# Performance work log

Hardware: AMD Instinct MI355X
Metric: run time of the kernel (lower is better)

The kernel has to match this reference:

```python
import jax, jax.numpy as jnp
import numpy as np

L, NH, D, FF, NL, NP = 6, 8, 256, 1024, 4, 4
HD = D // NH
B, Q0 = 4, 1000
SIZES = [(128, 128), (64, 64), (32, 32), (16, 16)]
KEEP_RATIO = 0.5


def _ln(x, w, b, eps=1e-5):
    mu = x.mean(-1, keepdims=True)
    var = ((x - mu) ** 2).mean(-1, keepdims=True)
    return (x - mu) * jax.lax.rsqrt(var + eps) * w + b


def _mha(q, k, v, in_w, in_b, out_w, out_b):
    # torch nn.MultiheadAttention (batch_first, eval mode => no dropout)
    Bq, Qn, _ = q.shape
    wq, wk, wv = jnp.split(in_w, 3, axis=0)
    bq, bk, bv = jnp.split(in_b, 3, axis=0)
    proj = lambda x, w, bb: (x @ w.T + bb).reshape(Bq, -1, NH, HD).transpose(0, 2, 1, 3)
    qh, kh, vh = proj(q, wq, bq), proj(k, wk, bk), proj(v, wv, bv)
    scores = jnp.einsum('bhqd,bhkd->bhqk', qh, kh) * (1.0 / np.float32(np.sqrt(HD)))
    a = jax.nn.softmax(scores, axis=-1)
    o = jnp.einsum('bhqk,bhkd->bhqd', a, vh).transpose(0, 2, 1, 3).reshape(Bq, Qn, D)
    return o @ out_w.T + out_b


def _bilinear(feat, grid):
    # feat [B,NH,HD,H,W]; grid [B,NH,Q,P,2] (x,y) in [-1,1]
    # matches F.grid_sample(mode='bilinear', padding_mode='zeros', align_corners=True)
    Bf, nh, hd, H, W = feat.shape
    gx = (grid[..., 0] + 1.0) * 0.5 * (W - 1)
    gy = (grid[..., 1] + 1.0) * 0.5 * (H - 1)
    x0, y0 = jnp.floor(gx), jnp.floor(gy)
    flat = feat.reshape(Bf, nh, hd, H * W)
    Qn, P = grid.shape[2], grid.shape[3]

    def corner(xi, yi, w):
        valid = (xi >= 0) & (xi <= W - 1) & (yi >= 0) & (yi <= H - 1)
        idx = (jnp.clip(yi, 0, H - 1).astype(jnp.int32) * W
               + jnp.clip(xi, 0, W - 1).astype(jnp.int32)).reshape(Bf, nh, Qn * P)
        vals = jnp.take_along_axis(flat, jnp.broadcast_to(idx[:, :, None, :], (Bf, nh, hd, Qn * P)), axis=3)
        vals = vals.reshape(Bf, nh, hd, Qn, P)
        return vals * (w * valid)[:, :, None]

    wx1, wy1 = gx - x0, gy - y0
    return (corner(x0, y0, (1 - wx1) * (1 - wy1)) + corner(x0 + 1, y0, wx1 * (1 - wy1))
            + corner(x0, y0 + 1, (1 - wx1) * wy1) + corner(x0 + 1, y0 + 1, wx1 * wy1))


def _msdeform(query, feats, ref, off_w, off_b, aw_w, aw_b, out_w, out_b):
    Bq, Qn, _ = query.shape
    off = jnp.tanh((query @ off_w.T + off_b).reshape(Bq, Qn, NH, NL, NP, 2))
    attn = jax.nn.softmax((query @ aw_w.T + aw_b).reshape(Bq, Qn, NH, NL * NP), axis=3)
    attn = attn.reshape(Bq, Qn, NH, NL, NP)
    ref_grid = ref * 2.0 - 1.0  # [B,Q,2]
    agg = 0.0
    for lvl, feat in enumerate(feats):
        fh = feat.reshape(Bq, NH, HD, feat.shape[2], feat.shape[3])
        grid = ref_grid[:, None, :, None, :] + off[:, :, :, lvl].transpose(0, 2, 1, 3, 4)  # [B,NH,Q,NP,2]
        sampled = _bilinear(fh, grid)                     # [B,NH,HD,Q,NP]
        w = attn[:, :, :, lvl].transpose(0, 2, 1, 3)      # [B,NH,Q,NP]
        agg = agg + (sampled * w[:, :, None]).sum(-1)     # [B,NH,HD,Q]
    out = agg.transpose(0, 3, 1, 2).reshape(Bq, Qn, D)
    return out @ out_w.T + out_b, attn


def setup_inputs() -> dict:
    key = jax.random.key(0)
    ks = iter(jax.random.split(key, 64))
    nrm = lambda shape, s=0.02: jax.random.normal(next(ks), shape, jnp.float32) * s
    inp = {
        'query_objects': nrm((B, Q0, D), 1.0),
        'query_embed': nrm((B, Q0, D), 1.0),
    }
    for i, (H, W) in enumerate(SIZES):
        inp[f'feat{i}'] = nrm((B, D, H, W), 1.0)
    inp.update(
        sa_in_w=nrm((L, 3 * D, D)), sa_in_b=jnp.zeros((L, 3 * D)),
        sa_out_w=nrm((L, D, D)), sa_out_b=jnp.zeros((L, D)),
        off_w=nrm((L, NH * NL * NP * 2, D)), off_b=nrm((L, NH * NL * NP * 2), 0.1),
        aw_w=nrm((L, NH * NL * NP, D)), aw_b=jnp.zeros((L, NH * NL * NP)),
        ca_out_w=nrm((L, D, D)), ca_out_b=jnp.zeros((L, D)),
        ff_w1=nrm((L, FF, D)), ff_b1=jnp.zeros((L, FF)),
        ff_w2=nrm((L, D, FF)), ff_b2=jnp.zeros((L, D)),
        nsa_w=jnp.ones((L, D)), nsa_b=jnp.zeros((L, D)),
        nca_w=jnp.ones((L, D)), nca_b=jnp.zeros((L, D)),
        nff_w=jnp.ones((L, D)), nff_b=jnp.zeros((L, D)),
        ref_w1=nrm((D, D)), ref_b1=jnp.zeros((D,)),
        ref_w2=nrm((2, D)), ref_b2=jnp.zeros((2,)),
        score_w=nrm((1, D)), score_b=jnp.zeros((1,)),
        refine_w=nrm((2, D)), refine_b=jnp.zeros((2,)),
    )
    return inp


def reference(query_objects, query_embed, feat0, feat1, feat2, feat3,
              sa_in_w, sa_in_b, sa_out_w, sa_out_b,
              off_w, off_b, aw_w, aw_b, ca_out_w, ca_out_b,
              ff_w1, ff_b1, ff_w2, ff_b2,
              nsa_w, nsa_b, nca_w, nca_b, nff_w, nff_b,
              ref_w1, ref_b1, ref_w2, ref_b2,
              score_w, score_b, refine_w, refine_b):
    feats = [feat0, feat1, feat2, feat3]
    out, q_embed = query_objects, query_embed
    h = jax.nn.relu(q_embed @ ref_w1.T + ref_b1)
    ref_points = jax.nn.sigmoid(h @ ref_w2.T + ref_b2)  # [B,Q,2]
    outputs, attns = [], []
    for i in range(L):
        sa_in = _ln(out, nsa_w[i], nsa_b[i])
        sa_out = _mha(sa_in + q_embed, sa_in + q_embed, sa_in,
                      sa_in_w[i], sa_in_b[i], sa_out_w[i], sa_out_b[i])
        out = out + sa_out
        ca_in = _ln(out, nca_w[i], nca_b[i])
        ca_out, attn = _msdeform(ca_in + q_embed, feats, ref_points,
                                 off_w[i], off_b[i], aw_w[i], aw_b[i], ca_out_w[i], ca_out_b[i])
        out = out + ca_out
        ff_in = _ln(out, nff_w[i], nff_b[i])
        out = out + (jax.nn.relu(ff_in @ ff_w1[i].T + ff_b1[i]) @ ff_w2[i].T + ff_b2[i])
        delta = jnp.tanh(out @ refine_w.T + refine_b) * 0.5
        ref_points = jnp.clip(ref_points + delta, 0.0, 1.0)
        outputs.append(out)
        attns.append(attn)
        if i < L - 1:
            Qn = out.shape[1]
            keep = max(16, int(Qn * KEEP_RATIO))
            scores = jax.nn.sigmoid((jax.lax.stop_gradient(out) @ score_w.T + score_b)[..., 0])
            _, idx = jax.lax.top_k(scores, keep)
            out = jnp.take_along_axis(out, idx[:, :, None], axis=1)
            q_embed = jnp.take_along_axis(q_embed, idx[:, :, None], axis=1)
            ref_points = jnp.take_along_axis(ref_points, idx[:, :, None], axis=1)
    return tuple(outputs) + tuple(attns)
```

## Files before the change

### kernel.cpp

```cpp
#include <hip/hip_runtime.h>
#include <hip/hip_bf16.h>

#define BB 4
#define DD 256

typedef unsigned long long u64;
typedef long long s64;
typedef unsigned int u32;

__device__ __forceinline__ float sigm(float x) { return 1.0f / (1.0f + expf(-x)); }

__global__ void k_ln(const float* __restrict__ x, const float* __restrict__ w,
                     const float* __restrict__ b, float* __restrict__ ln) {
    int row = blockIdx.x, tid = threadIdx.x;
    float v = x[(size_t)row * DD + tid];
    __shared__ float sred[4];
    float s = v;
#pragma unroll
    for (int o = 32; o > 0; o >>= 1) s += __shfl_down(s, o);
    if ((tid & 63) == 0) sred[tid >> 6] = s;
    __syncthreads();
    float mu = (sred[0] + sred[1] + sred[2] + sred[3]) * (1.0f / 256.0f);
    __syncthreads();
    float d = v - mu;
    float s2 = d * d;
#pragma unroll
    for (int o = 32; o > 0; o >>= 1) s2 += __shfl_down(s2, o);
    if ((tid & 63) == 0) sred[tid >> 6] = s2;
    __syncthreads();
    float var = (sred[0] + sred[1] + sred[2] + sred[3]) * (1.0f / 256.0f);
    float r = rsqrtf(var + 1e-5f);
    ln[(size_t)row * DD + tid] = d * r * w[tid] + b[tid];
}

template <int ACT, int RES>
__device__ __forceinline__ void gemm_core(float (*As)[16][64], float (*Ws)[16][64],
                                          const float* __restrict__ A, const float* __restrict__ Pe, int pe,
                                          const float* __restrict__ W, const float* __restrict__ bias,
                                          const float* __restrict__ Rm, float* __restrict__ C,
                                          float* __restrict__ C2,
                                          int M, int N, int K, int row0, int col0) {
    int tid = threadIdx.x;
    int tx = tid & 15, ty = tid >> 4;
    int lm = tid >> 2, lk = (tid & 3) * 4;
    float acc[4][4] = {{0.f}};
    int ar = row0 + lm;
    const float* Arow = A + (size_t)ar * K + lk;
    const float* Prow = pe ? (Pe + (size_t)ar * K + lk) : nullptr;
    const float* Wrow = W + (size_t)(col0 + lm) * K + lk;
    float4 av = make_float4(0.f, 0.f, 0.f, 0.f), wv;
    if (ar < M) {
        av = *(const float4*)(Arow);
        if (pe) { float4 pv = *(const float4*)(Prow); av.x += pv.x; av.y += pv.y; av.z += pv.z; av.w += pv.w; }
    }
    wv = *(const float4*)(Wrow);
    As[0][lk + 0][lm] = av.x; As[0][lk + 1][lm] = av.y; As[0][lk + 2][lm] = av.z; As[0][lk + 3][lm] = av.w;
    Ws[0][lk + 0][lm] = wv.x; Ws[0][lk + 1][lm] = wv.y; Ws[0][lk + 2][lm] = wv.z; Ws[0][lk + 3][lm] = wv.w;
    __syncthreads();
    int nb = K >> 4;
    for (int t = 0; t < nb; t++) {
        int cur = t & 1, nxt = cur ^ 1;
        bool more = (t + 1 < nb);
        if (more) {
            int k0 = (t + 1) << 4;
            av = make_float4(0.f, 0.f, 0.f, 0.f);
            if (ar < M) {
                av = *(const float4*)(Arow + k0);
                if (pe) { float4 pv = *(const float4*)(Prow + k0); av.x += pv.x; av.y += pv.y; av.z += pv.z; av.w += pv.w; }
            }
            wv = *(const float4*)(Wrow + k0);
        }
#pragma unroll
        for (int kk = 0; kk < 16; kk++) {
            float4 a = *(const float4*)&As[cur][kk][ty << 2];
            float4 w = *(const float4*)&Ws[cur][kk][tx << 2];
            acc[0][0] += a.x * w.x; acc[0][1] += a.x * w.y; acc[0][2] += a.x * w.z; acc[0][3] += a.x * w.w;
            acc[1][0] += a.y * w.x; acc[1][1] += a.y * w.y; acc[1][2] += a.y * w.z; acc[1][3] += a.y * w.w;
            acc[2][0] += a.z * w.x; acc[2][1] += a.z * w.y; acc[2][2] += a.z * w.z; acc[2][3] += a.z * w.w;
            acc[3][0] += a.w * w.x; acc[3][1] += a.w * w.y; acc[3][2] += a.w * w.z; acc[3][3] += a.w * w.w;
        }
        if (more) {
            As[nxt][lk + 0][lm] = av.x; As[nxt][lk + 1][lm] = av.y; As[nxt][lk + 2][lm] = av.z; As[nxt][lk + 3][lm] = av.w;
            Ws[nxt][lk + 0][lm] = wv.x; Ws[nxt][lk + 1][lm] = wv.y; Ws[nxt][lk + 2][lm] = wv.z; Ws[nxt][lk + 3][lm] = wv.w;
        }
        __syncthreads();
    }
#pragma unroll
    for (int i2 = 0; i2 < 4; i2++) {
        int r = row0 + (ty << 2) + i2;
        if (r >= M) continue;
        int cc = col0 + (tx << 2);
        float4 v;
        v.x = acc[i2][0] + bias[cc + 0];
        v.y = acc[i2][1] + bias[cc + 1];
        v.z = acc[i2][2] + bias[cc + 2];
        v.w = acc[i2][3] + bias[cc + 3];
        if (ACT == 1) { v.x = fmaxf(v.x, 0.f); v.y = fmaxf(v.y, 0.f); v.z = fmaxf(v.z, 0.f); v.w = fmaxf(v.w, 0.f); }
        if (RES == 1) {
            float4 rm = *(const float4*)(Rm + (size_t)r * N + cc);
            v.x += rm.x; v.y += rm.y; v.z += rm.z; v.w += rm.w;
        }
        *(float4*)(C + (size_t)r * N + cc) = v;
        if (C2) *(float4*)(C2 + (size_t)r * N + cc) = v;
    }
}

template <int ACT, int RES, int PE>
__global__ __launch_bounds__(256) void k_gemm(const float* __restrict__ A, const float* __restrict__ Pe,
                                              const float* __restrict__ W, const float* __restrict__ bias,
                                              const float* __restrict__ Rm, float* __restrict__ C,
                                              int M, int N, int K) {
    __shared__ float As[2][16][64];
    __shared__ float Ws[2][16][64];
    gemm_core<ACT, RES>(As, Ws, A, Pe, PE, W, bias, Rm, C, nullptr, M, N, K, blockIdx.y * 64, blockIdx.x * 64);
}

__global__ __launch_bounds__(256) void k_gemm_st2(const float* __restrict__ A, const float* __restrict__ W,
                                                  const float* __restrict__ bias, const float* __restrict__ Rm,
                                                  float* __restrict__ C, float* __restrict__ C2,
                                                  int M, int N, int K) {
    __shared__ float As[2][16][64];
    __shared__ float Ws[2][16][64];
    gemm_core<0, 1>(As, Ws, A, nullptr, 0, W, bias, Rm, C, C2, M, N, K, blockIdx.y * 64, blockIdx.x * 64);
}

__global__ __launch_bounds__(256) void k_gemm_qkv(const float* __restrict__ A, const float* __restrict__ Pe,
                                                  const float* __restrict__ Wqkv, const float* __restrict__ bqkv,
                                                  float* __restrict__ Cq, float* __restrict__ Ck, float* __restrict__ Cv,
                                                  int M, int K) {
    __shared__ float As[2][16][64];
    __shared__ float Ws[2][16][64];
    int z = blockIdx.z;
    const float* W = Wqkv + (size_t)z * 256 * K;
    const float* bias = bqkv + z * 256;
    float* C = (z == 0) ? Cq : (z == 1) ? Ck : Cv;
    gemm_core<0, 0>(As, Ws, A, Pe, (z < 2) ? 1 : 0, W, bias, nullptr, C, nullptr, M, 256, K,
                    blockIdx.y * 64, blockIdx.x * 64);
}

__global__ __launch_bounds__(256) void k_gemm_offaw(const float* __restrict__ A, const float* __restrict__ Pe,
                                                    const float* __restrict__ Woff, const float* __restrict__ boff,
                                                    const float* __restrict__ Waw, const float* __restrict__ baw,
                                                    float* __restrict__ Coff, float* __restrict__ Caw,
                                                    int M, int K) {
    __shared__ float As[2][16][64];
    __shared__ float Ws[2][16][64];
    int z = blockIdx.z;
    int N = (z == 0) ? 256 : 128;
    if ((int)(blockIdx.x * 64) >= N) return;
    gemm_core<0, 0>(As, Ws, A, Pe, 1, (z == 0) ? Woff : Waw, (z == 0) ? boff : baw, nullptr,
                    (z == 0) ? Coff : Caw, nullptr, M, N, K, blockIdx.y * 64, blockIdx.x * 64);
}

#define MHA_DOT8(SREG, JJ)                                                       \
    {                                                                            \
        _Pragma("unroll")                                                        \
        for (int u = 0; u < 8; u++) SREG[u] = 0.f;                               \
        _Pragma("unroll")                                                        \
        for (int c4 = 0; c4 < 8; c4++) {                                         \
            float q0 = qv[c4 * 4 + 0], q1 = qv[c4 * 4 + 1];                      \
            float q2 = qv[c4 * 4 + 2], q3 = qv[c4 * 4 + 3];                      \
            _Pragma("unroll")                                                    \
            for (int u = 0; u < 8; u++) {                                        \
                float4 k4 = *(const float4*)&Ks[(JJ) + u][c4 * 4];               \
                SREG[u] += q0 * k4.x; SREG[u] += q1 * k4.y;                      \
                SREG[u] += q2 * k4.z; SREG[u] += q3 * k4.w;                      \
            }                                                                    \
        }                                                                        \
    }

__global__ __launch_bounds__(64) void k_mha(const float* __restrict__ Qb, const float* __restrict__ Kb,
                                            const float* __restrict__ Vb, float* __restrict__ Ob, int Qn) {
    int bh = blockIdx.y;
    int b = bh >> 3, h = bh & 7;
    int lane = threadIdx.x;
    int qi = blockIdx.x * 64 + lane;
    __shared__ float Ks[64][36];
    __shared__ float Vs[64][36];
    float qv[32];
    float acc[32];
#pragma unroll
    for (int c = 0; c < 32; c++) acc[c] = 0.f;
    float m = -INFINITY, l = 0.f;
    const float scale = 0.17677669529663687f;
    bool active = qi < Qn;
    if (active) {
        const float4* qp = (const float4*)(Qb + ((size_t)(b * Qn + qi)) * DD + h * 32);
#pragma unroll
        for (int c4 = 0; c4 < 8; c4++) {
            float4 t = qp[c4];
            qv[c4 * 4 + 0] = t.x * scale; qv[c4 * 4 + 1] = t.y * scale;
            qv[c4 * 4 + 2] = t.z * scale; qv[c4 * 4 + 3] = t.w * scale;
        }
    } else {
#pragma unroll
        for (int c = 0; c < 32; c++) qv[c] = 0.f;
    }
    for (int k0 = 0; k0 < Qn; k0 += 64) {
        int nk = Qn - k0; if (nk > 64) nk = 64;
        if (lane < nk) {
            const float4* kp = (const float4*)(Kb + ((size_t)(b * Qn + k0 + lane)) * DD + h * 32);
            const float4* vp = (const float4*)(Vb + ((size_t)(b * Qn + k0 + lane)) * DD + h * 32);
#pragma unroll
            for (int c4 = 0; c4 < 8; c4++) {
                *(float4*)&Ks[lane][c4 * 4] = kp[c4];
                *(float4*)&Vs[lane][c4 * 4] = vp[c4];
            }
        }
        __syncthreads();
        int ng = nk >> 3;
        float scur[8], snxt[8];
        if (ng > 0) MHA_DOT8(scur, 0)
        for (int g = 0; g < ng; g++) {
            int jj = g << 3;
            bool morep = (g + 1 < ng);
            if (morep) MHA_DOT8(snxt, jj + 8)
            float mch[9];
            mch[0] = m;
#pragma unroll
            for (int u = 0; u < 8; u++) mch[u + 1] = fmaxf(mch[u], scur[u]);
            float e8[8];
#pragma unroll
            for (int u = 0; u < 8; u++) e8[u] = expf(fminf(mch[u] - scur[u], scur[u] - mch[u]));
            float sc8[8], p8[8];
#pragma unroll
            for (int u = 0; u < 8; u++) {
                bool gt = scur[u] > mch[u];
                sc8[u] = gt ? e8[u] : 1.0f;
                p8[u] = gt ? 1.0f : e8[u];
                l = l * sc8[u] + p8[u];
            }
            m = mch[8];
            float4 vc[8], vn[8];
#pragma unroll
            for (int c4 = 0; c4 < 8; c4++) vc[c4] = *(const float4*)&Vs[jj][c4 * 4];
#pragma unroll
            for (int u = 0; u < 8; u++) {
                if (u < 7) {
#pragma unroll
                    for (int c4 = 0; c4 < 8; c4++) vn[c4] = *(const float4*)&Vs[jj + u + 1][c4 * 4];
                }
                float sc = sc8[u], p = p8[u];
#pragma unroll
                for (int c4 = 0; c4 < 8; c4++) {
                    acc[c4 * 4 + 0] = acc[c4 * 4 + 0] * sc + p * vc[c4].x;
                    acc[c4 * 4 + 1] = acc[c4 * 4 + 1] * sc + p * vc[c4].y;
                    acc[c4 * 4 + 2] = acc[c4 * 4 + 2] * sc + p * vc[c4].z;
                    acc[c4 * 4 + 3] = acc[c4 * 4 + 3] * sc + p * vc[c4].w;
                }
                if (u < 7) {
#pragma unroll
                    for (int c4 = 0; c4 < 8; c4++) vc[c4] = vn[c4];
                }
            }
            if (morep) {
#pragma unroll
                for (int u = 0; u < 8; u++) scur[u] = snxt[u];
            }
        }
        for (int j = ng << 3; j < nk; j++) {
            float sv = 0.f;
#pragma unroll
            for (int c4 = 0; c4 < 8; c4++) {
                float4 k4 = *(const float4*)&Ks[j][c4 * 4];
                sv += qv[c4 * 4 + 0] * k4.x; sv += qv[c4 * 4 + 1] * k4.y;
                sv += qv[c4 * 4 + 2] * k4.z; sv += qv[c4 * 4 + 3] * k4.w;
            }
            float mn = fmaxf(m, sv);
            float e = expf(fminf(m - sv, sv - m));
            bool gt = sv > m;
            float sc = gt ? e : 1.0f;
            float p = gt ? 1.0f : e;
            l = l * sc + p;
            m = mn;
#pragma unroll
            for (int c4 = 0; c4 < 8; c4++) {
                float4 v4 = *(const float4*)&Vs[j][c4 * 4];
                acc[c4 * 4 + 0] = acc[c4 * 4 + 0] * sc + p * v4.x;
                acc[c4 * 4 + 1] = acc[c4 * 4 + 1] * sc + p * v4.y;
                acc[c4 * 4 + 2] = acc[c4 * 4 + 2] * sc + p * v4.z;
                acc[c4 * 4 + 3] = acc[c4 * 4 + 3] * sc + p * v4.w;
            }
        }
        __syncthreads();
    }
    if (active) {
        float inv = 1.0f / l;
        float* op = Ob + ((size_t)(b * Qn + qi)) * DD + h * 32;
#pragma unroll
        for (int c4 = 0; c4 < 8; c4++) {
            float4 o;
            o.x = acc[c4 * 4 + 0] * inv; o.y = acc[c4 * 4 + 1] * inv;
            o.z = acc[c4 * 4 + 2] * inv; o.w = acc[c4 * 4 + 3] * inv;
            *(float4*)(op + c4 * 4) = o;
        }
    }
}

__global__ __launch_bounds__(256) void k_trfeat(const float* __restrict__ in, float* __restrict__ out, int HH) {
    __shared__ float t[32][65];
    int bh = blockIdx.y;
    int b = bh >> 3, h = bh & 7;
    int s0 = blockIdx.x * 64;
    int tid = threadIdx.x;
    const float* ip = in + ((size_t)(b * 256 + h * 32)) * HH + s0;
#pragma unroll
    for (int i = 0; i < 8; i++) {
        int idx = i * 256 + tid;
        int c = idx >> 6, s = idx & 63;
        t[c][s] = ip[(size_t)c * HH + s];
    }
    __syncthreads();
    float* op = out + ((size_t)bh * HH + s0) * 32;
#pragma unroll
    for (int i = 0; i < 8; i++) {
        int idx = i * 256 + tid;
        int s = idx >> 5, c = idx & 31;
        op[(size_t)s * 32 + c] = t[c][s];
    }
}

__device__ __forceinline__ float d_samp(const float* fp, int W, int H, int x, int y) {
    if (x < 0 || x > W - 1 || y < 0 || y > H - 1) return 0.f;
    return fp[y * W + x];
}
__device__ __forceinline__ float d_bil(const float* fp, int W, int H, float gx, float gy) {
    float fx = (gx + 1.0f) * 0.5f * (float)(W - 1);
    float fy = (gy + 1.0f) * 0.5f * (float)(H - 1);
    float x0f = floorf(fx), y0f = floorf(fy);
    int x0 = (int)x0f, y0 = (int)y0f;
    float wx = fx - x0f, wy = fy - y0f;
    float v00 = d_samp(fp, W, H, x0, y0);
    float v10 = d_samp(fp, W, H, x0 + 1, y0);
    float v01 = d_samp(fp, W, H, x0, y0 + 1);
    float v11 = d_samp(fp, W, H, x0 + 1, y0 + 1);
    return v00 * (1.f - wx) * (1.f - wy) + v10 * wx * (1.f - wy) + v01 * (1.f - wx) * wy + v11 * wx * wy;
}
__device__ __forceinline__ float d_samp32(const float* fp, int W, int H, int x, int y) {
    if (x < 0 || x > W - 1 || y < 0 || y > H - 1) return 0.f;
    return fp[(size_t)(y * W + x) * 32];
}
__device__ __forceinline__ float d_bil32(const float* fp, int W, int H, float gx, float gy) {
    float fx = (gx + 1.0f) * 0.5f * (float)(W - 1);
    float fy = (gy + 1.0f) * 0.5f * (float)(H - 1);
    float x0f = floorf(fx), y0f = floorf(fy);
    int x0 = (int)x0f, y0 = (int)y0f;
    float wx = fx - x0f, wy = fy - y0f;
    float v00 = d_samp32(fp, W, H, x0, y0);
    float v10 = d_samp32(fp, W, H, x0 + 1, y0);
    float v01 = d_samp32(fp, W, H, x0, y0 + 1);
    float v11 = d_samp32(fp, W, H, x0 + 1, y0 + 1);
    return v00 * (1.f - wx) * (1.f - wy) + v10 * wx * (1.f - wy) + v01 * (1.f - wx) * wy + v11 * wx * wy;
}

template <int TR>
__global__ __launch_bounds__(256) void k_deform(const float* __restrict__ offL, const float* __restrict__ awL,
                                                const float* __restrict__ ref,
                                                const float* __restrict__ f0, const float* __restrict__ f1,
                                                const float* __restrict__ f2, const float* __restrict__ f3,
                                                float* __restrict__ caf, float* __restrict__ attn_out,
                                                int Qn) {
    int row = blockIdx.x;
    int b = row / Qn;
    int tid = threadIdx.x;
    __shared__ float attn_s[8][16];
    __shared__ float off_s[8][16][2];
    __shared__ float rxy[2];
    if (tid < 8) {
        int h = tid;
        const float* ap = awL + (size_t)row * 128 + h * 16;
        float mx = -INFINITY;
        float e[16];
#pragma unroll
        for (int j = 0; j < 16; j++) mx = fmaxf(mx, ap[j]);
        float ssum = 0.f;
#pragma unroll
        for (int j = 0; j < 16; j++) { e[j] = expf(ap[j] - mx); ssum += e[j]; }
        float inv = 1.0f / ssum;
        float* ao = attn_out + (size_t)row * 128 + h * 16;
#pragma unroll
        for (int j = 0; j < 16; j++) {
            float p = e[j] * inv;
            attn_s[h][j] = p;
            ao[j] = p;
        }
        const float* op = offL + (size_t)row * 256 + h * 32;
#pragma unroll
        for (int j = 0; j < 16; j++) {
            off_s[h][j][0] = tanhf(op[j * 2 + 0]);
            off_s[h][j][1] = tanhf(op[j * 2 + 1]);
        }
    }
    if (tid == 8) {
        rxy[0] = ref[(size_t)row * 2 + 0] * 2.f - 1.f;
        rxy[1] = ref[(size_t)row * 2 + 1] * 2.f - 1.f;
    }
    __syncthreads();
    int h = tid >> 5, c = tid & 31;
    float agg = 0.f;
#pragma unroll
    for (int l = 0; l < 4; l++) {
        const int H = 128 >> l;
        const float* base = (l == 0 ? f0 : l == 1 ? f1 : l == 2 ? f2 : f3);
        const float* fp;
        if (TR) fp = base + ((size_t)(b * 8 + h) * (H * H)) * 32 + c;
        else    fp = base + (size_t)(b * DD + h * 32 + c) * H * H;
#pragma unroll
        for (int p = 0; p < 4; p++) {
            int j = l * 4 + p;
            float sv;
            if (TR) sv = d_bil32(fp, H, H, rxy[0] + off_s[h][j][0], rxy[1] + off_s[h][j][1]);
            else    sv = d_bil(fp, H, H, rxy[0] + off_s[h][j][0], rxy[1] + off_s[h][j][1]);
            agg += attn_s[h][j] * sv;
        }
    }
    caf[(size_t)row * DD + h * 32 + c] = agg;
}

__global__ __launch_bounds__(64) void k_refinit(const float* __restrict__ hbuf, const float* __restrict__ w2,
                                                const float* __restrict__ b2, float* __restrict__ ref) {
    int row = blockIdx.x, lane = threadIdx.x;
    const float* hp = hbuf + (size_t)row * DD;
    float s0 = 0.f, s1 = 0.f;
#pragma unroll
    for (int d = 0; d < 4; d++) {
        int dd = lane + d * 64;
        float v = hp[dd];
        s0 += v * w2[dd];
        s1 += v * w2[DD + dd];
    }
#pragma unroll
    for (int o = 32; o > 0; o >>= 1) { s0 += __shfl_down(s0, o); s1 += __shfl_down(s1, o); }
    if (lane == 0) {
        ref[(size_t)row * 2 + 0] = sigm(s0 + b2[0]);
        ref[(size_t)row * 2 + 1] = sigm(s1 + b2[1]);
    }
}

__global__ __launch_bounds__(64) void k_refsc(const float* __restrict__ out, const float* __restrict__ rw,
                                              const float* __restrict__ rb, float* __restrict__ ref,
                                              const float* __restrict__ sw, const float* __restrict__ sb,
                                              float* __restrict__ score) {
    int row = blockIdx.x, lane = threadIdx.x;
    const float* op = out + (size_t)row * DD;
    float s0 = 0.f, s1 = 0.f;
#pragma unroll
    for (int d = 0; d < 4; d++) {
        int dd = lane + d * 64;
        float v = op[dd];
        s0 += v * rw[dd];
        s1 += v * rw[DD + dd];
    }
#pragma unroll
    for (int o = 32; o > 0; o >>= 1) { s0 += __shfl_down(s0, o); s1 += __shfl_down(s1, o); }
    if (lane == 0) {
        float r0 = ref[(size_t)row * 2 + 0] + tanhf(s0 + rb[0]) * 0.5f;
        float r1 = ref[(size_t)row * 2 + 1] + tanhf(s1 + rb[1]) * 0.5f;
        ref[(size_t)row * 2 + 0] = fminf(fmaxf(r0, 0.f), 1.f);
        ref[(size_t)row * 2 + 1] = fminf(fmaxf(r1, 0.f), 1.f);
        float s = sb[0];
        for (int d = 0; d < DD; d++) s += op[d] * sw[d];
        score[row] = sigm(s);
    }
}

__global__ __launch_bounds__(256) void k_topk(const float* __restrict__ score, int* __restrict__ idx,
                                              int Qn, int PAD, int keep) {
    __shared__ u64 keys[1024];
    int b = blockIdx.x, tid = threadIdx.x;
    for (int q = tid; q < PAD; q += 256) {
        u64 key;
        if (q < Qn) {
            u32 u = __float_as_uint(score[b * Qn + q]);
            u = (u & 0x80000000u) ? ~u : (u | 0x80000000u);
            u32 hi = ~u;
            key = (((u64)hi) << 32) | (u32)q;
        } else {
            key = 0xFFFFFFFFFFFFFFFFULL;
        }
        keys[q] = key;
    }
    __syncthreads();
    for (int k = 2; k <= PAD; k <<= 1) {
        for (int j = k >> 1; j > 0; j >>= 1) {
            for (int i = tid; i < PAD; i += 256) {
                int ij = i ^ j;
                if (ij > i) {
                    bool up = ((i & k) == 0);
                    u64 a = keys[i], c = keys[ij];
                    if ((a > c) == up) { keys[i] = c; keys[ij] = a; }
                }
            }
            __syncthreads();
        }
    }
    for (int t = tid; t < keep; t += 256) idx[b * keep + t] = (int)(keys[t] & 0xFFFFFFFFu);
}

__global__ __launch_bounds__(256) void k_gather(const float* __restrict__ osrc, const float* __restrict__ esrc,
                                                const float* __restrict__ rsrc, const int* __restrict__ idx,
                                                float* __restrict__ oT, float* __restrict__ eT,
                                                float* __restrict__ rT, int Qin, int keep) {
    int j = blockIdx.x;
    int b = j / keep;
    int src = idx[j];
    int tid = threadIdx.x;
    size_t srow = (size_t)(b * Qin + src), drow = (size_t)j;
    oT[drow * DD + tid] = osrc[srow * DD + tid];
    eT[drow * DD + tid] = esrc[srow * DD + tid];
    if (tid < 2) rT[drow * 2 + tid] = rsrc[srow * 2 + tid];
}

__global__ __launch_bounds__(256) void k_copyback(const float* __restrict__ oT, const float* __restrict__ eT,
                                                  const float* __restrict__ rT, float* __restrict__ o,
                                                  float* __restrict__ e, float* __restrict__ r) {
    int row = blockIdx.x, tid = threadIdx.x;
    o[(size_t)row * DD + tid] = oT[(size_t)row * DD + tid];
    e[(size_t)row * DD + tid] = eT[(size_t)row * DD + tid];
    if (tid < 2) r[(size_t)row * 2 + tid] = rT[(size_t)row * 2 + tid];
}

extern "C" void kernel_launch(void* const* d_in, const int* in_sizes, int n_in,
                              void* d_out, int out_size, void* d_ws, size_t ws_size,
                              hipStream_t stream) {
    (void)in_sizes; (void)n_in; (void)out_size;
    const float* q_obj = (const float*)d_in[0];
    const float* q_emb = (const float*)d_in[1];
    const float* feat0 = (const float*)d_in[2];
    const float* feat1 = (const float*)d_in[3];
    const float* feat2 = (const float*)d_in[4];
    const float* feat3 = (const float*)d_in[5];
    const float* sa_in_w = (const float*)d_in[6];
    const float* sa_in_b = (const float*)d_in[7];
    const float* sa_out_w = (const float*)d_in[8];
    const float* sa_out_b = (const float*)d_in[9];
    const float* off_w = (const float*)d_in[10];
    const float* off_b = (const float*)d_in[11];
    const float* aw_w = (const float*)d_in[12];
    const float* aw_b = (const float*)d_in[13];
    const float* ca_out_w = (const float*)d_in[14];
    const float* ca_out_b = (const float*)d_in[15];
    const float* ff_w1 = (const float*)d_in[16];
    const float* ff_b1 = (const float*)d_in[17];
    const float* ff_w2 = (const float*)d_in[18];
    const float* ff_b2 = (const float*)d_in[19];
    const float* nsa_w = (const float*)d_in[20];
    const float* nsa_b = (const float*)d_in[21];
    const float* nca_w = (const float*)d_in[22];
    const float* nca_b = (const float*)d_in[23];
    const float* nff_w = (const float*)d_in[24];
    const float* nff_b = (const float*)d_in[25];
    const float* ref_w1 = (const float*)d_in[26];
    const float* ref_b1 = (const float*)d_in[27];
    const float* ref_w2 = (const float*)d_in[28];
    const float* ref_b2 = (const float*)d_in[29];
    const float* score_w = (const float*)d_in[30];
    const float* score_b = (const float*)d_in[31];
    const float* refine_w = (const float*)d_in[32];
    const float* refine_b = (const float*)d_in[33];

    float* outf = (float*)d_out;
    float* ws = (float*)d_ws;
    const int RD = 4000 * 256;
    float* f_out = ws;
    float* f_emb = ws + RD;
    float* f_ln  = ws + 2 * RD;
    float* sc0   = ws + 3 * RD;
    float* sc1   = ws + 4 * RD;
    float* sc2   = ws + 5 * RD;
    float* f_ref = ws + 6 * RD;
    float* f_sc  = ws + 6 * RD + 8000;
    int*   i_idx = (int*)(ws + 6 * RD + 12032);
    float* f_tr  = ws + 6 * RD + 16384;
    static const s64 tr_ofs[4] = {0, 16777216, 20971520, 22020096};
    const size_t tr_need_bytes = ((size_t)(6 * RD + 16384) + 22282240ULL) * 4ULL;
    const bool use_tr = ws_size >= tr_need_bytes;

    static const int Qs[6] = {1000, 500, 250, 125, 62, 31};
    static const s64 out_ofs[6] = {0, 1024000, 1536000, 1792000, 1920000, 1983488};
    static const s64 attn_ofs[6] = {2015232, 2527232, 2783232, 2911232, 2975232, 3006976};

    hipMemcpyAsync(f_out, q_obj, (size_t)RD * 4, hipMemcpyDeviceToDevice, stream);
    hipMemcpyAsync(f_emb, q_emb, (size_t)RD * 4, hipMemcpyDeviceToDevice, stream);

    if (use_tr) {
        k_trfeat<<<dim3(16384 / 64, 32), 256, 0, stream>>>(feat0, f_tr + tr_ofs[0], 16384);
        k_trfeat<<<dim3(4096 / 64, 32), 256, 0, stream>>>(feat1, f_tr + tr_ofs[1], 4096);
        k_trfeat<<<dim3(1024 / 64, 32), 256, 0, stream>>>(feat2, f_tr + tr_ofs[2], 1024);
        k_trfeat<<<dim3(256 / 64, 32), 256, 0, stream>>>(feat3, f_tr + tr_ofs[3], 256);
    }

    k_gemm<1, 0, 0><<<dim3(4, 63), 256, 0, stream>>>(f_emb, nullptr, ref_w1, ref_b1, nullptr, f_ln, 4000, 256, 256);
    k_refinit<<<4000, 64, 0, stream>>>(f_ln, ref_w2, ref_b2, f_ref);

    for (int i = 0; i < 6; i++) {
        const int Q = Qs[i];
        const int R = BB * Q;
        const int gy = (R + 63) / 64;
        const float* siw = sa_in_w + (size_t)i * 768 * 256;
        const float* sib = sa_in_b + (size_t)i * 768;

        k_ln<<<R, 256, 0, stream>>>(f_out, nsa_w + i * 256, nsa_b + i * 256, f_ln);
        k_gemm_qkv<<<dim3(4, gy, 3), 256, 0, stream>>>(f_ln, f_emb, siw, sib, sc0, sc1, sc2, R, 256);
        k_mha<<<dim3((Q + 63) / 64, 32), 64, 0, stream>>>(sc0, sc1, sc2, f_ln, Q);
        k_gemm<0, 1, 0><<<dim3(4, gy), 256, 0, stream>>>(f_ln, nullptr, sa_out_w + (size_t)i * 65536,
                                                         sa_out_b + i * 256, f_out, f_out, R, 256, 256);

        k_ln<<<R, 256, 0, stream>>>(f_out, nca_w + i * 256, nca_b + i * 256, f_ln);
        k_gemm_offaw<<<dim3(4, gy, 2), 256, 0, stream>>>(f_ln, f_emb, off_w + (size_t)i * 65536, off_b + i * 256,
                                                         aw_w + (size_t)i * 32768, aw_b + i * 128, sc0, sc1, R, 256);
        if (use_tr)
            k_deform<1><<<R, 256, 0, stream>>>(sc0, sc1, f_ref, f_tr + tr_ofs[0], f_tr + tr_ofs[1],
                                               f_tr + tr_ofs[2], f_tr + tr_ofs[3], sc2, outf + attn_ofs[i], Q);
        else
            k_deform<0><<<R, 256, 0, stream>>>(sc0, sc1, f_ref, feat0, feat1, feat2, feat3, sc2,
                                               outf + attn_ofs[i], Q);
        k_gemm<0, 1, 0><<<dim3(4, gy), 256, 0, stream>>>(sc2, nullptr, ca_out_w + (size_t)i * 65536,
                                                         ca_out_b + i * 256, f_out, f_out, R, 256, 256);

        k_ln<<<R, 256, 0, stream>>>(f_out, nff_w + i * 256, nff_b + i * 256, f_ln);
        for (int r0 = 0; r0 < R; r0 += 2000) {
            int mc = R - r0; if (mc > 2000) mc = 2000;
            int gyc = (mc + 63) / 64;
            k_gemm<1, 0, 0><<<dim3(16, gyc), 256, 0, stream>>>(f_ln + (size_t)r0 * 256, nullptr,
                                                               ff_w1 + (size_t)i * 262144, ff_b1 + i * 1024,
                                                               nullptr, sc0, mc, 1024, 256);
            k_gemm_st2<<<dim3(4, gyc), 256, 0, stream>>>(sc0, ff_w2 + (size_t)i * 262144,
                                                         ff_b2 + i * 256, f_out + (size_t)r0 * 256,
                                                         f_out + (size_t)r0 * 256,
                                                         outf + out_ofs[i] + (size_t)r0 * 256, mc, 256, 1024);
        }

        if (i < 5) {
            int keep = Qs[i + 1];
            int PAD = 1;
            while (PAD < Q) PAD <<= 1;
            k_refsc<<<R, 64, 0, stream>>>(f_out, refine_w, refine_b, f_ref, score_w, score_b, f_sc);
            k_topk<<<4, 256, 0, stream>>>(f_sc, i_idx, Q, PAD, keep);
            k_gather<<<4 * keep, 256, 0, stream>>>(f_out, f_emb, f_ref, i_idx, sc0, sc1, sc2, Q, keep);
            k_copyback<<<4 * keep, 256, 0, stream>>>(sc0, sc1, sc2, f_out, f_emb, f_ref);
        }
    }
}
```

Before: 2.351 ms.

## Materialize attention scores, unchunk FFN, and ping-pong buffers instead of copyback

Self-attention is split into two kernels. The first writes the full QK^T score matrix to a workspace buffer with a grid parallel over key tiles. The second runs an online softmax and the V accumulation from that buffer, prefetching the scores. The FFN runs as one GEMM pair over all rows using a larger hidden buffer instead of 2000-row chunks. After top-k, the gather writes into alternate buffers that are pointer-swapped, which removes the copyback kernel. All of this needs a much larger workspace, and it adds global-memory traffic for the score matrix (32 heads x Q^2 floats).

```diff
diff --git a/kernel.cpp b/kernel.cpp
--- a/kernel.cpp
+++ b/kernel.cpp
@@ -168,6 +168,162 @@
             }                                                                    \
         }                                                                        \
     }
+
+__global__ __launch_bounds__(64) void k_qk(const float* __restrict__ Qb, const float* __restrict__ Kb,
+                                           float* __restrict__ S, int Qn) {
+    int bh = blockIdx.z;
+    int b = bh >> 3, h = bh & 7;
+    int lane = threadIdx.x;
+    int qi = blockIdx.x * 64 + lane;
+    int j0 = blockIdx.y * 64;
+    __shared__ float Ks[64][36];
+    float qv[32];
+    const float scale = 0.17677669529663687f;
+    bool active = qi < Qn;
+    if (active) {
+        const float4* qp = (const float4*)(Qb + ((size_t)(b * Qn + qi)) * DD + h * 32);
+#pragma unroll
+        for (int c4 = 0; c4 < 8; c4++) {
+            float4 t = qp[c4];
+            qv[c4 * 4 + 0] = t.x * scale; qv[c4 * 4 + 1] = t.y * scale;
+            qv[c4 * 4 + 2] = t.z * scale; qv[c4 * 4 + 3] = t.w * scale;
+        }
+    } else {
+#pragma unroll
+        for (int c = 0; c < 32; c++) qv[c] = 0.f;
+    }
+    int nj = Qn - j0; if (nj > 64) nj = 64;
+    if (lane < nj) {
+        const float4* kp = (const float4*)(Kb + ((size_t)(b * Qn + j0 + lane)) * DD + h * 32);
+#pragma unroll
+        for (int c4 = 0; c4 < 8; c4++) *(float4*)&Ks[lane][c4 * 4] = kp[c4];
+    }
+    __syncthreads();
+    float* Sp = S + (size_t)bh * Qn * Qn;
+    float scur[8];
+    for (int g = 0; g < 8; g++) {
+        int jj = g << 3;
+        if (jj >= nj) break;
+        MHA_DOT8(scur, jj)
+#pragma unroll
+        for (int u = 0; u < 8; u++) {
+            int j = j0 + jj + u;
+            if (active && j < Qn) Sp[(size_t)j * Qn + qi] = scur[u];
+        }
+    }
+}
+
+__global__ __launch_bounds__(64) void k_mha_s(const float* __restrict__ S, const float* __restrict__ Vb,
+                                              float* __restrict__ Ob, int Qn) {
+    int bh = blockIdx.y;
+    int b = bh >> 3, h = bh & 7;
+    int lane = threadIdx.x;
+    int qi = blockIdx.x * 64 + lane;
+    __shared__ float Vs[64][36];
+    float acc[32];
+#pragma unroll
+    for (int c = 0; c < 32; c++) acc[c] = 0.f;
+    float m = -INFINITY, l = 0.f;
+    bool active = qi < Qn;
+    int qs = active ? qi : 0;
+    const float* Sq = S + (size_t)bh * Qn * Qn + qs;
+    int ng = Qn >> 3;
+    float scur[8], snxt[8];
+#pragma unroll
+    for (int u = 0; u < 8; u++) scur[u] = Sq[(size_t)u * Qn];
+    int gg = 0;
+    for (int k0 = 0; k0 < Qn; k0 += 64) {
+        int nk = Qn - k0; if (nk > 64) nk = 64;
+        if (lane < nk) {
+            const float4* vp = (const float4*)(Vb + ((size_t)(b * Qn + k0 + lane)) * DD + h * 32);
+#pragma unroll
+            for (int c4 = 0; c4 < 8; c4++) *(float4*)&Vs[lane][c4 * 4] = vp[c4];
+        }
+        __syncthreads();
+        int gl = nk >> 3;
+        for (int g2 = 0; g2 < gl; g2++, gg++) {
+            int jj = g2 << 3;
+            bool morep = (gg + 1 < ng);
+            if (morep) {
+                const float* Sn = Sq + (size_t)(k0 + jj + 8) * Qn;
+#pragma unroll
+                for (int u = 0; u < 8; u++) snxt[u] = Sn[(size_t)u * Qn];
+            }
+            float mch[9];
+            mch[0] = m;
+#pragma unroll
+            for (int u = 0; u < 8; u++) mch[u + 1] = fmaxf(mch[u], scur[u]);
+            float e8[8];
+#pragma unroll
+            for (int u = 0; u < 8; u++) e8[u] = expf(fminf(mch[u] - scur[u], scur[u] - mch[u]));
+            float sc8[8], p8[8];
+#pragma unroll
+            for (int u = 0; u < 8; u++) {
+                bool gt = scur[u] > mch[u];
+                sc8[u] = gt ? e8[u] : 1.0f;
+                p8[u] = gt ? 1.0f : e8[u];
+                l = l * sc8[u] + p8[u];
+            }
+            m = mch[8];
+            float4 vc[8], vn[8];
+#pragma unroll
+            for (int c4 = 0; c4 < 8; c4++) vc[c4] = *(const float4*)&Vs[jj][c4 * 4];
+#pragma unroll
+            for (int u = 0; u < 8; u++) {
+                if (u < 7) {
+#pragma unroll
+                    for (int c4 = 0; c4 < 8; c4++) vn[c4] = *(const float4*)&Vs[jj + u + 1][c4 * 4];
+                }
+                float sc = sc8[u], p = p8[u];
+#pragma unroll
+                for (int c4 = 0; c4 < 8; c4++) {
+                    acc[c4 * 4 + 0] = acc[c4 * 4 + 0] * sc + p * vc[c4].x;
+                    acc[c4 * 4 + 1] = acc[c4 * 4 + 1] * sc + p * vc[c4].y;
+                    acc[c4 * 4 + 2] = acc[c4 * 4 + 2] * sc + p * vc[c4].z;
+                    acc[c4 * 4 + 3] = acc[c4 * 4 + 3] * sc + p * vc[c4].w;
+                }
+                if (u < 7) {
+#pragma unroll
+                    for (int c4 = 0; c4 < 8; c4++) vc[c4] = vn[c4];
+                }
+            }
+            if (morep) {
+#pragma unroll
+                for (int u = 0; u < 8; u++) scur[u] = snxt[u];
+            }
+        }
+        for (int j = gl << 3; j < nk; j++) {
+            float sv = Sq[(size_t)(k0 + j) * Qn];
+            float mn = fmaxf(m, sv);
+            float e = expf(fminf(m - sv, sv - m));
+            bool gt = sv > m;
+            float sc = gt ? e : 1.0f;
+            float p = gt ? 1.0f : e;
+            l = l * sc + p;
+            m = mn;
+#pragma unroll
+            for (int c4 = 0; c4 < 8; c4++) {
+                float4 v4 = *(const float4*)&Vs[j][c4 * 4];
+                acc[c4 * 4 + 0] = acc[c4 * 4 + 0] * sc + p * v4.x;
+                acc[c4 * 4 + 1] = acc[c4 * 4 + 1] * sc + p * v4.y;
+                acc[c4 * 4 + 2] = acc[c4 * 4 + 2] * sc + p * v4.z;
+                acc[c4 * 4 + 3] = acc[c4 * 4 + 3] * sc + p * v4.w;
+            }
+        }
+        __syncthreads();
+    }
+    if (active) {
+        float inv = 1.0f / l;
+        float* op = Ob + ((size_t)(b * Qn + qi)) * DD + h * 32;
+#pragma unroll
+        for (int c4 = 0; c4 < 8; c4++) {
+            float4 o;
+            o.x = acc[c4 * 4 + 0] * inv; o.y = acc[c4 * 4 + 1] * inv;
+            o.z = acc[c4 * 4 + 2] * inv; o.w = acc[c4 * 4 + 3] * inv;
+            *(float4*)(op + c4 * 4) = o;
+        }
+    }
+}
 
 __global__ __launch_bounds__(64) void k_mha(const float* __restrict__ Qb, const float* __restrict__ Kb,
                                             const float* __restrict__ Vb, float* __restrict__ Ob, int Qn) {
@@ -575,6 +731,13 @@
     static const s64 tr_ofs[4] = {0, 16777216, 20971520, 22020096};
     const size_t tr_need_bytes = ((size_t)(6 * RD + 16384) + 22282240ULL) * 4ULL;
     const bool use_tr = ws_size >= tr_need_bytes;
+    float* Sbuf   = f_tr + 22282240;
+    float* f_hid  = Sbuf + 32000000;
+    float* f_out2 = f_hid + 4096000;
+    float* f_emb2 = f_out2 + 1024000;
+    float* f_ref2 = f_emb2 + 1024000;
+    const size_t ext_need_bytes = ((size_t)28442624ULL + 32000000ULL + 4096000ULL + 1024000ULL + 1024000ULL + 8000ULL) * 4ULL;
+    const bool use_ext = use_tr && (ws_size >= ext_need_bytes);
 
     static const int Qs[6] = {1000, 500, 250, 125, 62, 31};
     static const s64 out_ofs[6] = {0, 1024000, 1536000, 1792000, 1920000, 1983488};
@@ -592,6 +755,9 @@
 
     k_gemm<1, 0, 0><<<dim3(4, 63), 256, 0, stream>>>(f_emb, nullptr, ref_w1, ref_b1, nullptr, f_ln, 4000, 256, 256);
     k_refinit<<<4000, 64, 0, stream>>>(f_ln, ref_w2, ref_b2, f_ref);
+
+    float* po = f_out; float* pe = f_emb; float* pr = f_ref;
+    float* qo = f_out2; float* qe = f_emb2; float* qr = f_ref2;
 
     for (int i = 0; i < 6; i++) {
         const int Q = Qs[i];
@@ -600,45 +766,68 @@
         const float* siw = sa_in_w + (size_t)i * 768 * 256;
         const float* sib = sa_in_b + (size_t)i * 768;
 
-        k_ln<<<R, 256, 0, stream>>>(f_out, nsa_w + i * 256, nsa_b + i * 256, f_ln);
-        k_gemm_qkv<<<dim3(4, gy, 3), 256, 0, stream>>>(f_ln, f_emb, siw, sib, sc0, sc1, sc2, R, 256);
-        k_mha<<<dim3((Q + 63) / 64, 32), 64, 0, stream>>>(sc0, sc1, sc2, f_ln, Q);
+        k_ln<<<R, 256, 0, stream>>>(po, nsa_w + i * 256, nsa_b + i * 256, f_ln);
+        k_gemm_qkv<<<dim3(4, gy, 3), 256, 0, stream>>>(f_ln, pe, siw, sib, sc0, sc1, sc2, R, 256);
+        if (use_ext) {
+            int qt = (Q + 63) / 64;
+            k_qk<<<dim3(qt, qt, 32), 64, 0, stream>>>(sc0, sc1, Sbuf, Q);
+            k_mha_s<<<dim3(qt, 32), 64, 0, stream>>>(Sbuf, sc2, f_ln, Q);
+        } else {
+            k_mha<<<dim3((Q + 63) / 64, 32), 64, 0, stream>>>(sc0, sc1, sc2, f_ln, Q);
+        }
         k_gemm<0, 1, 0><<<dim3(4, gy), 256, 0, stream>>>(f_ln, nullptr, sa_out_w + (size_t)i * 65536,
-                                                         sa_out_b + i * 256, f_out, f_out, R, 256, 256);
-
-        k_ln<<<R, 256, 0, stream>>>(f_out, nca_w + i * 256, nca_b + i * 256, f_ln);
-        k_gemm_offaw<<<dim3(4, gy, 2), 256, 0, stream>>>(f_ln, f_emb, off_w + (size_t)i * 65536, off_b + i * 256,
+                                                         sa_out_b + i * 256, po, po, R, 256, 256);
+
+        k_ln<<<R, 256, 0, stream>>>(po, nca_w + i * 256, nca_b + i * 256, f_ln);
+        k_gemm_offaw<<<dim3(4, gy, 2), 256, 0, stream>>>(f_ln, pe, off_w + (size_t)i * 65536, off_b + i * 256,
                                                          aw_w + (size_t)i * 32768, aw_b + i * 128, sc0, sc1, R, 256);
         if (use_tr)
-            k_deform<1><<<R, 256, 0, stream>>>(sc0, sc1, f_ref, f_tr + tr_ofs[0], f_tr + tr_ofs[1],
+            k_deform<1><<<R, 256, 0, stream>>>(sc0, sc1, pr, f_tr + tr_ofs[0], f_tr + tr_ofs[1],
                                                f_tr + tr_ofs[2], f_tr + tr_ofs[3], sc2, outf + attn_ofs[i], Q);
         else
-            k_deform<0><<<R, 256, 0, stream>>>(sc0, sc1, f_ref, feat0, feat1, feat2, feat3, sc2,
+            k_deform<0><<<R, 256, 0, stream>>>(sc0, sc1, pr, feat0, feat1, feat2, feat3, sc2,
                                                outf + attn_ofs[i], Q);
         k_gemm<0, 1, 0><<<dim3(4, gy), 256, 0, stream>>>(sc2, nullptr, ca_out_w + (size_t)i * 65536,
-                                                         ca_out_b + i * 256, f_out, f_out, R, 256, 256);
-
-        k_ln<<<R, 256, 0, stream>>>(f_out, nff_w + i * 256, nff_b + i * 256, f_ln);
-        for (int r0 = 0; r0 < R; r0 += 2000) {
-            int mc = R - r0; if (mc > 2000) mc = 2000;
-            int gyc = (mc + 63) / 64;
-            k_gemm<1, 0, 0><<<dim3(16, gyc), 256, 0, stream>>>(f_ln + (size_t)r0 * 256, nullptr,
-                                                               ff_w1 + (size_t)i * 262144, ff_b1 + i * 1024,
-                                                               nullptr, sc0, mc, 1024, 256);
-            k_gemm_st2<<<dim3(4, gyc), 256, 0, stream>>>(sc0, ff_w2 + (size_t)i * 262144,
-                                                         ff_b2 + i * 256, f_out + (size_t)r0 * 256,
-                                                         f_out + (size_t)r0 * 256,
-                                                         outf + out_ofs[i] + (size_t)r0 * 256, mc, 256, 1024);
+                                                         ca_out_b + i * 256, po, po, R, 256, 256);
+
+        k_ln<<<R, 256, 0, stream>>>(po, nff_w + i * 256, nff_b + i * 256, f_ln);
+        if (use_ext) {
+            k_gemm<1, 0, 0><<<dim3(16, gy), 256, 0, stream>>>(f_ln, nullptr,
+                                                              ff_w1 + (size_t)i * 262144, ff_b1 + i * 1024,
+                                                              nullptr, f_hid, R, 1024, 256);
+            k_gemm_st2<<<dim3(4, gy), 256, 0, stream>>>(f_hid, ff_w2 + (size_t)i * 262144,
+                                                        ff_b2 + i * 256, po, po,
+                                                        outf + out_ofs[i], R, 256, 1024);
+        } else {
+            for (int r0 = 0; r0 < R; r0 += 2000) {
+                int mc = R - r0; if (mc > 2000) mc = 2000;
+                int gyc = (mc + 63) / 64;
+                k_gemm<1, 0, 0><<<dim3(16, gyc), 256, 0, stream>>>(f_ln + (size_t)r0 * 256, nullptr,
+                                                                   ff_w1 + (size_t)i * 262144, ff_b1 + i * 1024,
+                                                                   nullptr, sc0, mc, 1024, 256);
+                k_gemm_st2<<<dim3(4, gyc), 256, 0, stream>>>(sc0, ff_w2 + (size_t)i * 262144,
+                                                             ff_b2 + i * 256, po + (size_t)r0 * 256,
+                                                             po + (size_t)r0 * 256,
+                                                             outf + out_ofs[i] + (size_t)r0 * 256, mc, 256, 1024);
+            }
         }
 
         if (i < 5) {
             int keep = Qs[i + 1];
             int PAD = 1;
             while (PAD < Q) PAD <<= 1;
-            k_refsc<<<R, 64, 0, stream>>>(f_out, refine_w, refine_b, f_ref, score_w, score_b, f_sc);
+            k_refsc<<<R, 64, 0, stream>>>(po, refine_w, refine_b, pr, score_w, score_b, f_sc);
             k_topk<<<4, 256, 0, stream>>>(f_sc, i_idx, Q, PAD, keep);
-            k_gather<<<4 * keep, 256, 0, stream>>>(f_out, f_emb, f_ref, i_idx, sc0, sc1, sc2, Q, keep);
-            k_copyback<<<4 * keep, 256, 0, stream>>>(sc0, sc1, sc2, f_out, f_emb, f_ref);
-        }
-    }
-}
+            if (use_ext) {
+                k_gather<<<4 * keep, 256, 0, stream>>>(po, pe, pr, i_idx, qo, qe, qr, Q, keep);
+                float* t;
+                t = po; po = qo; qo = t;
+                t = pe; pe = qe; qe = t;
+                t = pr; pr = qr; qr = t;
+            } else {
+                k_gather<<<4 * keep, 256, 0, stream>>>(po, pe, pr, i_idx, sc0, sc1, sc2, Q, keep);
+                k_copyback<<<4 * keep, 256, 0, stream>>>(sc0, sc1, sc2, po, pe, pr);
+            }
+        }
+    }
+}
```

After: 2.117 ms. 1.11x faster.
